# Kernel optimization log

Hardware: AMD Instinct MI355X
Metric: run time of the kernel (lower is better)

## Reference

```python
import jax, jax.numpy as jnp
import numpy as np

P = 8.0  # Lp exponent of the distance neuron (finite-p stage of l_inf-dist training)


def _patches(t, k, stride, pad):
    # [B, Cin, H, W] -> [B, Cin*k*k, H', W'], feature dim ordered channel-major
    return jax.lax.conv_general_dilated_patches(
        t, (k, k), (stride, stride), [(pad, pad), (pad, pad)])


def _lp(d):
    # d: [B, Cout, Cin*k*k, H', W'] nonnegative -> Lp norm over patch dim
    return jnp.power(jnp.sum(jnp.power(d, P), axis=2), 1.0 / P)


def norm_dist_conv(x, l, u, w, stride, pad):
    # Lp-distance "convolution": y[b,o,i,j] = || patch(x)[b,:,i,j] - w[o,:] ||_p
    # mean_normalize=True: zero-center each output unit's weight vector
    Cout, Cin, k, _ = w.shape
    wf = w.reshape(Cout, -1)
    wf = wf - jnp.mean(wf, axis=1, keepdims=True)
    wb = wf[None, :, :, None, None]                      # [1, Cout, Ckk, 1, 1]
    px = _patches(x, k, stride, pad)[:, None]            # [B, 1, Ckk, H', W']
    pl = _patches(l, k, stride, pad)[:, None]
    pu = _patches(u, k, stride, pad)[:, None]
    y = _lp(jnp.abs(px - wb))
    # interval bounds of |x_j - w_j| given x_j in [l_j, u_j], then monotone Lp
    dl = jnp.maximum(jnp.maximum(pl - wb, wb - pu), 0.0)
    du = jnp.maximum(jnp.abs(pl - wb), jnp.abs(pu - wb))
    return y, _lp(dl), _lp(du)


def bound_relu(x, l, u):
    # ReLU is monotone: apply elementwise to value and both bounds
    return jax.nn.relu(x), jax.nn.relu(l), jax.nn.relu(u)


def setup_inputs() -> dict:
    key = jax.random.key(0)
    k1, k2, k3 = jax.random.split(key, 3)
    B, C, H, W = 4, 32, 32, 32
    eps = 0.1  # l_inf perturbation radius
    x = jax.random.normal(k1, (B, C, H, W), dtype=jnp.float32)
    lower = x - eps
    upper = x + eps
    scale = 1.0 / np.sqrt(C * 9)
    weight1 = jax.random.normal(k2, (C, C, 3, 3), dtype=jnp.float32) * scale
    weight2 = jax.random.normal(k3, (C, C, 3, 3), dtype=jnp.float32) * scale
    return {"x": x, "lower": lower, "upper": upper,
            "weight1": weight1, "weight2": weight2}


def reference(x, lower, upper, weight1, weight2):
    # conv1 (stride=1, pad=1) -> BoundReLU -> conv2 -> residual add -> BoundReLU
    o = norm_dist_conv(x, lower, upper, weight1, 1, 1)
    o = bound_relu(*o)
    o = norm_dist_conv(*o, weight2, 1, 1)
    out = (o[0] + x, o[1] + lower, o[2] + upper)  # identity shortcut (stride=1, in==out)
    out = bound_relu(*out)
    return jnp.stack(out)  # [3, B, C, H, W]: (value, lower, upper)
```

## Files before the change

kernel.cpp:

```cpp
#include <hip/hip_runtime.h>
#include <hip/hip_bf16.h>

#define NB 4
#define NC 32
#define NH 32
#define NW 32
#define KK 288
#define PLANE (NB*NC*NH*NW)

template<bool STAGE2>
__global__ __launch_bounds__(256) void normdist_conv_k(
    const float* __restrict__ xb,
    const float* __restrict__ lb,
    const float* __restrict__ ub,
    const float* __restrict__ my,
    const float* __restrict__ ml,
    const float* __restrict__ mu,
    const float* __restrict__ wraw,
    float* __restrict__ oy, float* __restrict__ ol, float* __restrict__ ou,
    float* __restrict__ out)
{
    const int h   = blockIdx.x;
    const int cog = blockIdx.y;
    const int b   = blockIdx.z;
    const int tx  = threadIdx.x;
    const int ty  = threadIdx.y;
    const int tid = ty * 32 + tx;

    __shared__ float4 sP[NC*3*34];
    __shared__ float  sWf[8*NC*3*4];
    float4* sW4 = (float4*)sWf;

    for (int i = tid; i < 8*KK; i += 256) {
        const int co  = i / KK;
        const int rem = i - co*KK;
        const int c   = rem / 9;
        const int r9  = rem - c*9;
        const int r   = r9 / 3;
        const int kw  = r9 - r*3;
        sWf[((co*NC + c)*3 + r)*4 + kw] = wraw[(cog*8 + co)*KK + rem];
    }

    for (int i = tid; i < NC*3*34; i += 256) {
        const int c   = i / 102;
        const int rem = i - c*102;
        const int r   = rem / 34;
        const int col = rem - r*34;
        const int gh  = h + r - 1;
        const int gw  = col - 1;
        float vx = 0.0f, vl = 0.0f, vu = 0.0f;
        if ((unsigned)gh < NH && (unsigned)gw < NW) {
            const int g = ((b*NC + c)*NH + gh)*NW + gw;
            if (STAGE2) { vx = my[g]; vl = ml[g]; vu = mu[g]; }
            else        { vx = xb[g]; vl = lb[g]; vu = ub[g]; }
        }
        sP[i] = make_float4(vx, vl, vu, 0.0f);
    }
    __syncthreads();

    {
        const int co = tid >> 5;
        const int c  = tid & 31;
        float4 a0 = sW4[(co*NC + c)*3 + 0];
        float4 a1 = sW4[(co*NC + c)*3 + 1];
        float4 a2 = sW4[(co*NC + c)*3 + 2];
        float s = a0.x+a0.y+a0.z + a1.x+a1.y+a1.z + a2.x+a2.y+a2.z;
        #pragma unroll
        for (int off = 16; off > 0; off >>= 1) s += __shfl_xor(s, off, 32);
        const float mean = s * (1.0f / (float)KK);
        a0.x -= mean; a0.y -= mean; a0.z -= mean; a0.w = 0.0f;
        a1.x -= mean; a1.y -= mean; a1.z -= mean; a1.w = 0.0f;
        a2.x -= mean; a2.y -= mean; a2.z -= mean; a2.w = 0.0f;
        sW4[(co*NC + c)*3 + 0] = a0;
        sW4[(co*NC + c)*3 + 1] = a1;
        sW4[(co*NC + c)*3 + 2] = a2;
    }
    __syncthreads();

    float accY = 0.0f, accL = 0.0f, accU = 0.0f;

    auto tap = [&](float wv, float4 p) {
        const float d  = p.x - wv;
        const float d2 = d*d, d4 = d2*d2;
        accY = fmaf(d4, d4, accY);
        const float a  = p.y - wv;
        const float nb = wv - p.z;
        const float m  = fmaxf(fmaxf(a, nb), 0.0f);
        const float m2 = m*m, m4 = m2*m2;
        accL = fmaf(m4, m4, accL);
        const float a2 = a*a, q2 = nb*nb;
        const float mm2 = fmaxf(a2, q2);
        const float mm4 = mm2*mm2;
        accU = fmaf(mm4, mm4, accU);
    };

    #pragma unroll 4
    for (int c = 0; c < NC; ++c) {
        const float4 w0 = sW4[(ty*NC + c)*3 + 0];
        const float4 w1 = sW4[(ty*NC + c)*3 + 1];
        const float4 w2 = sW4[(ty*NC + c)*3 + 2];
        const int pb = c*3*34 + tx;
        const float4 p00 = sP[pb +   0], p01 = sP[pb +   1], p02 = sP[pb +   2];
        const float4 p10 = sP[pb +  34], p11 = sP[pb +  35], p12 = sP[pb +  36];
        const float4 p20 = sP[pb +  68], p21 = sP[pb +  69], p22 = sP[pb +  70];
        tap(w0.x, p00); tap(w0.y, p01); tap(w0.z, p02);
        tap(w1.x, p10); tap(w1.y, p11); tap(w1.z, p12);
        tap(w2.x, p20); tap(w2.y, p21); tap(w2.z, p22);
    }

    const float y  = sqrtf(sqrtf(sqrtf(accY)));
    const float dl = sqrtf(sqrtf(sqrtf(accL)));
    const float du = sqrtf(sqrtf(sqrtf(accU)));

    const int co = cog*8 + ty;
    const int o  = ((b*NC + co)*NH + h)*NW + tx;
    if (!STAGE2) {
        oy[o] = y; ol[o] = dl; ou[o] = du;
    } else {
        out[o]           = fmaxf(y  + xb[o], 0.0f);
        out[PLANE + o]   = fmaxf(dl + lb[o], 0.0f);
        out[2*PLANE + o] = fmaxf(du + ub[o], 0.0f);
    }
}

extern "C" void kernel_launch(void* const* d_in, const int* in_sizes, int n_in,
                              void* d_out, int out_size, void* d_ws, size_t ws_size,
                              hipStream_t stream)
{
    const float* x  = (const float*)d_in[0];
    const float* l  = (const float*)d_in[1];
    const float* u  = (const float*)d_in[2];
    const float* w1 = (const float*)d_in[3];
    const float* w2 = (const float*)d_in[4];
    float* ws = (float*)d_ws;
    float* my = ws;
    float* ml = my + PLANE;
    float* mu = ml + PLANE;
    float* out = (float*)d_out;

    dim3 blk(32, 8);
    dim3 grd(NH, 4, NB);
    normdist_conv_k<false><<<grd, blk, 0, stream>>>(x, l, u, nullptr, nullptr, nullptr,
                                                    w1, my, ml, mu, nullptr);
    normdist_conv_k<true ><<<grd, blk, 0, stream>>>(x, l, u, my, ml, mu,
                                                    w2, nullptr, nullptr, nullptr, out);
}
```

Measured before the change: 113.3 us.

## Split conv1 over input-channel halves and fuse the root into conv2 load

The first distance conv is split across two input-channel halves, each writing partial p-th power sums to workspace, doubling the block count for more parallelism. The second kernel sums the partials and applies the 8th root while loading its input tile, then finishes with the residual and ReLU. This trades extra workspace traffic, duplicated weight preparation and redundant root computations on halo elements for better CU utilisation in stage one.

```diff
diff --git a/kernel.cpp b/kernel.cpp
--- a/kernel.cpp
+++ b/kernel.cpp
@@ -1,5 +1,4 @@
 #include <hip/hip_runtime.h>
-#include <hip/hip_bf16.h>
 
 #define NB 4
 #define NC 32
@@ -7,30 +6,13 @@
 #define NW 32
 #define KK 288
 #define PLANE (NB*NC*NH*NW)
+#define CHALF 16
 
-template<bool STAGE2>
-__global__ __launch_bounds__(256) void normdist_conv_k(
-    const float* __restrict__ xb,
-    const float* __restrict__ lb,
-    const float* __restrict__ ub,
-    const float* __restrict__ my,
-    const float* __restrict__ ml,
-    const float* __restrict__ mu,
-    const float* __restrict__ wraw,
-    float* __restrict__ oy, float* __restrict__ ol, float* __restrict__ ou,
-    float* __restrict__ out)
+__device__ __forceinline__ float s3(float v) { return sqrtf(sqrtf(sqrtf(v))); }
+
+__device__ __forceinline__ void prep_weights_lds(
+        const float* __restrict__ wraw, int cog, int tid, float* __restrict__ sWf)
 {
-    const int h   = blockIdx.x;
-    const int cog = blockIdx.y;
-    const int b   = blockIdx.z;
-    const int tx  = threadIdx.x;
-    const int ty  = threadIdx.y;
-    const int tid = ty * 32 + tx;
-
-    __shared__ float4 sP[NC*3*34];
-    __shared__ float  sWf[8*NC*3*4];
-    float4* sW4 = (float4*)sWf;
-
     for (int i = tid; i < 8*KK; i += 256) {
         const int co  = i / KK;
         const int rem = i - co*KK;
@@ -40,25 +22,9 @@
         const int kw  = r9 - r*3;
         sWf[((co*NC + c)*3 + r)*4 + kw] = wraw[(cog*8 + co)*KK + rem];
     }
-
-    for (int i = tid; i < NC*3*34; i += 256) {
-        const int c   = i / 102;
-        const int rem = i - c*102;
-        const int r   = rem / 34;
-        const int col = rem - r*34;
-        const int gh  = h + r - 1;
-        const int gw  = col - 1;
-        float vx = 0.0f, vl = 0.0f, vu = 0.0f;
-        if ((unsigned)gh < NH && (unsigned)gw < NW) {
-            const int g = ((b*NC + c)*NH + gh)*NW + gw;
-            if (STAGE2) { vx = my[g]; vl = ml[g]; vu = mu[g]; }
-            else        { vx = xb[g]; vl = lb[g]; vu = ub[g]; }
-        }
-        sP[i] = make_float4(vx, vl, vu, 0.0f);
-    }
     __syncthreads();
-
     {
+        float4* sW4 = (float4*)sWf;
         const int co = tid >> 5;
         const int c  = tid & 31;
         float4 a0 = sW4[(co*NC + c)*3 + 0];
@@ -75,52 +41,134 @@
         sW4[(co*NC + c)*3 + 1] = a1;
         sW4[(co*NC + c)*3 + 2] = a2;
     }
+}
+
+__device__ __forceinline__ void tap(float wv, float4 p, float& aY, float& aL, float& aU)
+{
+    const float d  = p.x - wv;
+    const float d2 = d*d, d4 = d2*d2;
+    aY = fmaf(d4, d4, aY);
+    const float a  = p.y - wv;
+    const float nb = wv - p.z;
+    const float m  = fmaxf(fmaxf(a, nb), 0.0f);
+    const float m2 = m*m, m4 = m2*m2;
+    aL = fmaf(m4, m4, aL);
+    const float mm  = fmaxf(fabsf(a), fabsf(nb));
+    const float mm2 = mm*mm, mm4 = mm2*mm2;
+    aU = fmaf(mm4, mm4, aU);
+}
+
+__global__ __launch_bounds__(256, 4) void conv1_k(
+    const float* __restrict__ x,  const float* __restrict__ l,  const float* __restrict__ u,
+    const float* __restrict__ w1,
+    float* __restrict__ pY, float* __restrict__ pL, float* __restrict__ pU)
+{
+    const int h     = blockIdx.x;
+    const int cog   = blockIdx.y >> 1;
+    const int chalf = blockIdx.y & 1;
+    const int ch0   = chalf * CHALF;
+    const int b     = blockIdx.z;
+    const int tx    = threadIdx.x;
+    const int ty    = threadIdx.y;
+    const int tid   = ty*32 + tx;
+
+    __shared__ float4 sP[CHALF*3*34];
+    __shared__ float  sWf[8*NC*3*4];
+
+    prep_weights_lds(w1, cog, tid, sWf);
+
+    for (int i = tid; i < CHALF*3*34; i += 256) {
+        const int c   = i / 102;
+        const int rem = i - c*102;
+        const int r   = rem / 34;
+        const int col = rem - r*34;
+        const int gh  = h + r - 1;
+        const int gw  = col - 1;
+        float vx = 0.0f, vl = 0.0f, vu = 0.0f;
+        if ((unsigned)gh < NH && (unsigned)gw < NW) {
+            const int g = ((b*NC + ch0 + c)*NH + gh)*NW + gw;
+            vx = x[g]; vl = l[g]; vu = u[g];
+        }
+        sP[i] = make_float4(vx, vl, vu, 0.0f);
+    }
     __syncthreads();
 
-    float accY = 0.0f, accL = 0.0f, accU = 0.0f;
+    const float4* sW4 = (const float4*)sWf;
+    float aY = 0.0f, aL = 0.0f, aU = 0.0f;
 
-    auto tap = [&](float wv, float4 p) {
-        const float d  = p.x - wv;
-        const float d2 = d*d, d4 = d2*d2;
-        accY = fmaf(d4, d4, accY);
-        const float a  = p.y - wv;
-        const float nb = wv - p.z;
-        const float m  = fmaxf(fmaxf(a, nb), 0.0f);
-        const float m2 = m*m, m4 = m2*m2;
-        accL = fmaf(m4, m4, accL);
-        const float a2 = a*a, q2 = nb*nb;
-        const float mm2 = fmaxf(a2, q2);
-        const float mm4 = mm2*mm2;
-        accU = fmaf(mm4, mm4, accU);
-    };
-
-    #pragma unroll 4
-    for (int c = 0; c < NC; ++c) {
-        const float4 w0 = sW4[(ty*NC + c)*3 + 0];
-        const float4 w1 = sW4[(ty*NC + c)*3 + 1];
-        const float4 w2 = sW4[(ty*NC + c)*3 + 2];
-        const int pb = c*3*34 + tx;
-        const float4 p00 = sP[pb +   0], p01 = sP[pb +   1], p02 = sP[pb +   2];
-        const float4 p10 = sP[pb +  34], p11 = sP[pb +  35], p12 = sP[pb +  36];
-        const float4 p20 = sP[pb +  68], p21 = sP[pb +  69], p22 = sP[pb +  70];
-        tap(w0.x, p00); tap(w0.y, p01); tap(w0.z, p02);
-        tap(w1.x, p10); tap(w1.y, p11); tap(w1.z, p12);
-        tap(w2.x, p20); tap(w2.y, p21); tap(w2.z, p22);
+    #pragma unroll 2
+    for (int c = 0; c < CHALF; ++c) {
+        const float4 w0 = sW4[(ty*NC + ch0 + c)*3 + 0];
+        const float4 w1v = sW4[(ty*NC + ch0 + c)*3 + 1];
+        const float4 w2v = sW4[(ty*NC + ch0 + c)*3 + 2];
+        const int pb = c*102 + tx;
+        tap(w0.x,  sP[pb +  0], aY,aL,aU); tap(w0.y,  sP[pb +  1], aY,aL,aU); tap(w0.z,  sP[pb +  2], aY,aL,aU);
+        tap(w1v.x, sP[pb + 34], aY,aL,aU); tap(w1v.y, sP[pb + 35], aY,aL,aU); tap(w1v.z, sP[pb + 36], aY,aL,aU);
+        tap(w2v.x, sP[pb + 68], aY,aL,aU); tap(w2v.y, sP[pb + 69], aY,aL,aU); tap(w2v.z, sP[pb + 70], aY,aL,aU);
     }
-
-    const float y  = sqrtf(sqrtf(sqrtf(accY)));
-    const float dl = sqrtf(sqrtf(sqrtf(accL)));
-    const float du = sqrtf(sqrtf(sqrtf(accU)));
 
     const int co = cog*8 + ty;
     const int o  = ((b*NC + co)*NH + h)*NW + tx;
-    if (!STAGE2) {
-        oy[o] = y; ol[o] = dl; ou[o] = du;
-    } else {
-        out[o]           = fmaxf(y  + xb[o], 0.0f);
-        out[PLANE + o]   = fmaxf(dl + lb[o], 0.0f);
-        out[2*PLANE + o] = fmaxf(du + ub[o], 0.0f);
+    pY[chalf*PLANE + o] = aY;
+    pL[chalf*PLANE + o] = aL;
+    pU[chalf*PLANE + o] = aU;
+}
+
+__global__ __launch_bounds__(256) void conv2epi_k(
+    const float* __restrict__ pY, const float* __restrict__ pL, const float* __restrict__ pU,
+    const float* __restrict__ x,  const float* __restrict__ l,  const float* __restrict__ u,
+    const float* __restrict__ w2,
+    float* __restrict__ out)
+{
+    const int h   = blockIdx.x;
+    const int cog = blockIdx.y;
+    const int b   = blockIdx.z;
+    const int tx  = threadIdx.x;
+    const int ty  = threadIdx.y;
+    const int tid = ty*32 + tx;
+
+    __shared__ float4 sP[NC*3*34];
+    __shared__ float  sWf[8*NC*3*4];
+
+    prep_weights_lds(w2, cog, tid, sWf);
+
+    for (int i = tid; i < NC*3*34; i += 256) {
+        const int c   = i / 102;
+        const int rem = i - c*102;
+        const int r   = rem / 34;
+        const int col = rem - r*34;
+        const int gh  = h + r - 1;
+        const int gw  = col - 1;
+        float vx = 0.0f, vl = 0.0f, vu = 0.0f;
+        if ((unsigned)gh < NH && (unsigned)gw < NW) {
+            const int g = ((b*NC + c)*NH + gh)*NW + gw;
+            vx = s3(pY[g] + pY[PLANE + g]);
+            vl = s3(pL[g] + pL[PLANE + g]);
+            vu = s3(pU[g] + pU[PLANE + g]);
+        }
+        sP[i] = make_float4(vx, vl, vu, 0.0f);
     }
+    __syncthreads();
+
+    const float4* sW4 = (const float4*)sWf;
+    float aY = 0.0f, aL = 0.0f, aU = 0.0f;
+
+    #pragma unroll 2
+    for (int c = 0; c < NC; ++c) {
+        const float4 w0 = sW4[(ty*NC + c)*3 + 0];
+        const float4 w1v = sW4[(ty*NC + c)*3 + 1];
+        const float4 w2v = sW4[(ty*NC + c)*3 + 2];
+        const int pb = c*102 + tx;
+        tap(w0.x,  sP[pb +  0], aY,aL,aU); tap(w0.y,  sP[pb +  1], aY,aL,aU); tap(w0.z,  sP[pb +  2], aY,aL,aU);
+        tap(w1v.x, sP[pb + 34], aY,aL,aU); tap(w1v.y, sP[pb + 35], aY,aL,aU); tap(w1v.z, sP[pb + 36], aY,aL,aU);
+        tap(w2v.x, sP[pb + 68], aY,aL,aU); tap(w2v.y, sP[pb + 69], aY,aL,aU); tap(w2v.z, sP[pb + 70], aY,aL,aU);
+    }
+
+    const int co = cog*8 + ty;
+    const int o  = ((b*NC + co)*NH + h)*NW + tx;
+    out[o]           = fmaxf(s3(aY) + x[o], 0.0f);
+    out[PLANE + o]   = fmaxf(s3(aL) + l[o], 0.0f);
+    out[2*PLANE + o] = fmaxf(s3(aU) + u[o], 0.0f);
 }
 
 extern "C" void kernel_launch(void* const* d_in, const int* in_sizes, int n_in,
@@ -132,16 +180,13 @@
     const float* u  = (const float*)d_in[2];
     const float* w1 = (const float*)d_in[3];
     const float* w2 = (const float*)d_in[4];
-    float* ws = (float*)d_ws;
-    float* my = ws;
-    float* ml = my + PLANE;
-    float* mu = ml + PLANE;
+    float* ws  = (float*)d_ws;
+    float* p1Y = ws;
+    float* p1L = p1Y + 2*PLANE;
+    float* p1U = p1L + 2*PLANE;
     float* out = (float*)d_out;
 
     dim3 blk(32, 8);
-    dim3 grd(NH, 4, NB);
-    normdist_conv_k<false><<<grd, blk, 0, stream>>>(x, l, u, nullptr, nullptr, nullptr,
-                                                    w1, my, ml, mu, nullptr);
-    normdist_conv_k<true ><<<grd, blk, 0, stream>>>(x, l, u, my, ml, mu,
-                                                    w2, nullptr, nullptr, nullptr, out);
+    conv1_k   <<<dim3(NH, 8, NB), blk, 0, stream>>>(x, l, u, w1, p1Y, p1L, p1U);
+    conv2epi_k<<<dim3(NH, 4, NB), blk, 0, stream>>>(p1Y, p1L, p1U, x, l, u, w2, out);
 }
```

After: 111.7 us. Within noise of the previous version (-1.4%).
